# Performance work log

Hardware: AMD Instinct MI355X
Metric: run time of the kernel (lower is better)

## Reference

```python
import jax, jax.numpy as jnp
import numpy as np
from jax import lax

K = 3
PAD = 1


def setup_inputs() -> dict:
    key = jax.random.key(0)
    k1, k2, k3 = jax.random.split(key, 3)
    B, Cin, Cout, H, W = 4, 64, 64, 128, 128
    x = jax.random.normal(k1, (B, Cin, H, W), dtype=jnp.float32)
    # offset-predicting conv params (2*K*K output channels); small init keeps offsets modest
    offset_w = jax.random.normal(k2, (2 * K * K, Cin, K, K), dtype=jnp.float32) * 0.05
    offset_b = jnp.zeros((2 * K * K,), dtype=jnp.float32)
    # deformable conv weight/bias (module uses randn weight, zero bias)
    weight = jax.random.normal(k3, (Cout, Cin, K, K), dtype=jnp.float32) * 0.05
    bias = jnp.zeros((Cout,), dtype=jnp.float32)
    return {"x": x, "offset_w": offset_w, "offset_b": offset_b, "weight": weight, "bias": bias}


def _conv2d(x, w, b):
    y = lax.conv_general_dilated(x, w, window_strides=(1, 1),
                                 padding=((PAD, PAD), (PAD, PAD)),
                                 dimension_numbers=("NCHW", "OIHW", "NCHW"))
    return y + b[None, :, None, None]


def _bilinear_gather(x, py, px):
    # x: [B,C,H,W]; py,px: [B,KK,HO,WO] sample coords -> [B,C,KK,HO,WO], zeros outside
    B, C, H, W = x.shape
    y0 = jnp.floor(py)
    x0 = jnp.floor(px)
    ly = py - y0
    lx = px - x0
    y0i = y0.astype(jnp.int32)
    x0i = x0.astype(jnp.int32)
    xf = x.reshape(B, C, H * W)

    def corner(yi, xi, w):
        mask = ((yi >= 0) & (yi < H) & (xi >= 0) & (xi < W)).astype(x.dtype)
        lin = jnp.clip(yi, 0, H - 1) * W + jnp.clip(xi, 0, W - 1)  # [B,KK,HO,WO]
        g = jax.vmap(lambda xb, ib: xb[:, ib])(xf, lin)            # [B,C,KK,HO,WO]
        return g * (w * mask)[:, None]

    return (corner(y0i, x0i, (1 - ly) * (1 - lx))
            + corner(y0i, x0i + 1, (1 - ly) * lx)
            + corner(y0i + 1, x0i, ly * (1 - lx))
            + corner(y0i + 1, x0i + 1, ly * lx))


def reference(x, offset_w, offset_b, weight, bias):
    B, Cin, H, W = x.shape
    Cout = weight.shape[0]
    KK = K * K
    offset = _conv2d(x, offset_w, offset_b)            # [B, 2*KK, H, W]
    off = offset.reshape(B, KK, 2, H, W)               # torchvision layout: (dy, dx) per tap
    dy, dx = off[:, :, 0], off[:, :, 1]                # [B,KK,H,W]
    ki = (jnp.arange(KK) // K).astype(x.dtype)
    kj = (jnp.arange(KK) % K).astype(x.dtype)
    hs = jnp.arange(H, dtype=x.dtype)
    ws = jnp.arange(W, dtype=x.dtype)
    base_y = ki[:, None, None] + hs[None, :, None] - PAD   # [KK,H,1]
    base_x = kj[:, None, None] + ws[None, None, :] - PAD   # [KK,1,W]
    py = dy + base_y[None]                             # [B,KK,H,W]
    px = dx + base_x[None]
    sampled = _bilinear_gather(x, py, px)              # [B,Cin,KK,H,W]
    out = jnp.einsum("bckhw,ock->bohw", sampled, weight.reshape(Cout, Cin, KK))
    return out + bias[None, :, None, None]
```

## Files before the change

### kernel.cpp

```cpp
#include <hip/hip_runtime.h>

typedef _Float16 f16x8 __attribute__((ext_vector_type(8)));
typedef float f32x4 __attribute__((ext_vector_type(4)));

__device__ __forceinline__ f16x8 splat8(float v) {
  _Float16 h = (_Float16)v;
  return f16x8{h, h, h, h, h, h, h, h};
}

__global__ __launch_bounds__(256) void k_xtprep(const float* __restrict__ x,
                                                const float* __restrict__ wt,
                                                const float* __restrict__ ow,
                                                _Float16* __restrict__ xt,
                                                _Float16* __restrict__ wb,
                                                _Float16* __restrict__ owb) {
  __shared__ float tile[64 * 65];
  int blk = blockIdx.x;
  int t = threadIdx.x;
  if (blk < 1024) {
    int b = blk >> 8;
    int y = (blk >> 1) & 127;
    int w0 = (blk & 1) * 64;
    const float* xp = x + ((size_t)(b * 64) * 128 + y) * 128 + w0;
#pragma unroll
    for (int it = 0; it < 4; ++it) {
      int idx = it * 256 + t;
      int c = idx >> 4, q = idx & 15;
      float4 v = *(const float4*)(xp + (size_t)c * 16384 + q * 4);
      float* tp = &tile[c * 65 + q * 4];
      tp[0] = v.x; tp[1] = v.y; tp[2] = v.z; tp[3] = v.w;
    }
    __syncthreads();
#pragma unroll
    for (int it = 0; it < 2; ++it) {
      int idx = it * 256 + t;
      int w = idx >> 3, c8 = idx & 7;
      f16x8 o;
#pragma unroll
      for (int j = 0; j < 8; ++j) o[j] = (_Float16)tile[(c8 * 8 + j) * 65 + w];
      *(f16x8*)&xt[(((size_t)b * 128 + y) * 128 + w0 + w) * 64 + c8 * 8] = o;
    }
  } else {
    int i = (blk - 1024) * 256 + t;
    if (i < 36864) {
      int k = i >> 12, rem = i & 4095, o = rem >> 6, c = rem & 63;
      wb[i] = (_Float16)wt[(o * 64 + c) * 9 + k];
    } else if (i < 36864 + 18432) {
      int j = i - 36864;
      int k = j >> 11, rem = j & 2047, o = rem >> 6, c = rem & 63;
      float v = (o < 18) ? ow[(o * 64 + c) * 9 + k] : 0.0f;
      owb[j] = (_Float16)v;
    }
  }
}

__global__ __launch_bounds__(256, 4) void k_fused(
    const _Float16* __restrict__ xt, const _Float16* __restrict__ wb,
    const _Float16* __restrict__ owb, const float* __restrict__ ob,
    const float* __restrict__ bias, float* __restrict__ out) {
  __shared__ char lds[37728];
  _Float16* S = (_Float16*)lds;
  _Float16* WkL = (_Float16*)(lds + 9216);
  float* offL = (float*)(lds + 18432);
  _Float16* Xs = (_Float16*)lds;
  _Float16* owbkL = (_Float16*)(lds + 28512);

  int t = threadIdx.x;
  int lb = (blockIdx.x & 7) * 128 + (blockIdx.x >> 3);
  int w0 = (lb & 1) * 64;
  int h = (lb >> 1) & 127;
  int b = lb >> 8;

  int lane = t & 63, wid = t >> 6;
  int row = lane & 15, quad = lane >> 4;
  const _Float16* xb = xt + (size_t)b * 128 * 128 * 64;

#pragma unroll
  for (int it = 0; it < 8; ++it) {
    int idx8 = it * 256 + t;
    if (idx8 < 1584) {
      int c8 = idx8 & 7;
      int jr = idx8 >> 3;
      int jj = jr % 66;
      int ki = jr / 66;
      int gy = h - 1 + ki;
      int gx = w0 - 1 + jj;
      f16x8 v = {};
      if (((unsigned)gy < 128u) & ((unsigned)gx < 128u))
        v = *(const f16x8*)(xb + ((size_t)gy * 128 + gx) * 64 + c8 * 8);
      *(f16x8*)&Xs[(ki * 66 + jj) * 72 + c8 * 8] = v;
    } else if (idx8 < 1840) {
      int j = idx8 - 1584;
      int o = j >> 3, c8 = j & 7;
      *(f16x8*)&owbkL[o * 72 + c8 * 8] = *(const f16x8*)(owb + j * 8);
    }
  }
  __syncthreads();

  {
    int woA = (wid >> 1) * 16;
    int wpA = (wid & 1) * 32;
    f32x4 accA[2];
    accA[0] = f32x4{0.f, 0.f, 0.f, 0.f};
    accA[1] = f32x4{0.f, 0.f, 0.f, 0.f};
#pragma unroll
    for (int k = 0; k < 9; ++k) {
      if (k < 8) {
        int o = t >> 3, c8 = t & 7;
        *(f16x8*)&owbkL[((k + 1) & 1) * 2304 + o * 72 + c8 * 8] =
            *(const f16x8*)(owb + (k + 1) * 2048 + t * 8);
      }
      int ki = k / 3, kj = k % 3;
      const _Float16* ap = &owbkL[(k & 1) * 2304 + (woA + row) * 72 + quad * 8];
      f16x8 afr0 = *(const f16x8*)(ap);
      f16x8 afr1 = *(const f16x8*)(ap + 32);
#pragma unroll
      for (int n = 0; n < 2; ++n) {
        int j = wpA + n * 16 + row + kj;
        const _Float16* lp = &Xs[(ki * 66 + j) * 72 + quad * 8];
        f16x8 b0 = *(const f16x8*)(lp);
        f16x8 b1 = *(const f16x8*)(lp + 32);
        accA[n] = __builtin_amdgcn_mfma_f32_16x16x32_f16(afr0, b0, accA[n], 0, 0, 0);
        accA[n] = __builtin_amdgcn_mfma_f32_16x16x32_f16(afr1, b1, accA[n], 0, 0, 0);
      }
      __syncthreads();
    }
    int qr = quad * 4;
#pragma unroll
    for (int n = 0; n < 2; ++n) {
#pragma unroll
      for (int r = 0; r < 4; ++r) {
        int co = woA + qr + r;
        if (co < 18)
          offL[(wpA + n * 16 + row) * 20 + co] = accA[n][r] + ob[co];
      }
    }
  }
  __syncthreads();

  int pix = t >> 2, cg = t & 3;
  int w = w0 + pix;
  int woB = (wid >> 1) * 32, wpB = (wid & 1) * 32;

  f32x4 acc[2][2];
#pragma unroll
  for (int i = 0; i < 2; ++i)
#pragma unroll
    for (int j = 0; j < 2; ++j) acc[i][j] = f32x4{0.f, 0.f, 0.f, 0.f};

  for (int k = 0; k < 9; ++k) {
    {
      const f16x8* src = (const f16x8*)(wb + k * 4096);
#pragma unroll
      for (int r = 0; r < 2; ++r) {
        int idx8 = r * 256 + t;
        int o = idx8 >> 3, c8 = idx8 & 7;
        *(f16x8*)&WkL[o * 72 + c8 * 8] = src[idx8];
      }
    }
    {
      int ki = k / 3, kj = k % 3;
      float dy = offL[pix * 20 + 2 * k];
      float dx = offL[pix * 20 + 2 * k + 1];
      float py = dy + (float)(h + ki - 1);
      float pxf = dx + (float)(w + kj - 1);
      float fy = floorf(py), fx = floorf(pxf);
      float ly = py - fy, lx = pxf - fx;
      int y0 = (int)fy, x0 = (int)fx;
      int y1 = y0 + 1, x1 = x0 + 1;
      bool vy0 = (unsigned)y0 < 128u, vy1 = (unsigned)y1 < 128u;
      bool vx0 = (unsigned)x0 < 128u, vx1 = (unsigned)x1 < 128u;
      float w00 = (vy0 && vx0) ? (1.f - ly) * (1.f - lx) : 0.f;
      float w01 = (vy0 && vx1) ? (1.f - ly) * lx : 0.f;
      float w10 = (vy1 && vx0) ? ly * (1.f - lx) : 0.f;
      float w11 = (vy1 && vx1) ? ly * lx : 0.f;
      int yc0 = min(max(y0, 0), 127), yc1 = min(max(y1, 0), 127);
      int xc0 = min(max(x0, 0), 127), xc1 = min(max(x1, 0), 127);
      const _Float16* p00 = xb + (yc0 * 128 + xc0) * 64 + cg * 16;
      int dxo = (xc1 - xc0) * 64;
      int dyo = (yc1 - yc0) * 8192;
      f16x8 a0 = *(const f16x8*)(p00);
      f16x8 a1 = *(const f16x8*)(p00 + 8);
      f16x8 b0 = *(const f16x8*)(p00 + dxo);
      f16x8 b1 = *(const f16x8*)(p00 + dxo + 8);
      f16x8 c0v = *(const f16x8*)(p00 + dyo);
      f16x8 c1 = *(const f16x8*)(p00 + dyo + 8);
      f16x8 d0 = *(const f16x8*)(p00 + dyo + dxo);
      f16x8 d1 = *(const f16x8*)(p00 + dyo + dxo + 8);
      f16x8 W00 = splat8(w00), W01 = splat8(w01);
      f16x8 W10 = splat8(w10), W11 = splat8(w11);
      f16x8 s0 = W00 * a0 + W01 * b0 + W10 * c0v + W11 * d0;
      f16x8 s1 = W00 * a1 + W01 * b1 + W10 * c1 + W11 * d1;
      *(f16x8*)&S[pix * 72 + cg * 16] = s0;
      *(f16x8*)&S[pix * 72 + cg * 16 + 8] = s1;
    }
    __syncthreads();
    {
#pragma unroll
      for (int ks = 0; ks < 2; ++ks) {
        int c0 = ks * 32 + quad * 8;
        f16x8 afr[2], bfr[2];
#pragma unroll
        for (int mi = 0; mi < 2; ++mi)
          afr[mi] = *(const f16x8*)&WkL[(woB + mi * 16 + row) * 72 + c0];
#pragma unroll
        for (int ni = 0; ni < 2; ++ni)
          bfr[ni] = *(const f16x8*)&S[(wpB + ni * 16 + row) * 72 + c0];
#pragma unroll
        for (int mi = 0; mi < 2; ++mi)
#pragma unroll
          for (int ni = 0; ni < 2; ++ni)
            acc[mi][ni] = __builtin_amdgcn_mfma_f32_16x16x32_f16(
                afr[mi], bfr[ni], acc[mi][ni], 0, 0, 0);
      }
    }
    __syncthreads();
  }
  {
    int col = lane & 15;
    int qr = quad * 4;
#pragma unroll
    for (int mi = 0; mi < 2; ++mi) {
#pragma unroll
      for (int ni = 0; ni < 2; ++ni) {
#pragma unroll
        for (int r = 0; r < 4; ++r) {
          int o = woB + mi * 16 + qr + r;
          int pw = w0 + wpB + ni * 16 + col;
          out[(((size_t)b * 64 + o) * 128 + h) * 128 + pw] = acc[mi][ni][r] + bias[o];
        }
      }
    }
  }
}

extern "C" void kernel_launch(void* const* d_in, const int* in_sizes, int n_in,
                              void* d_out, int out_size, void* d_ws,
                              size_t ws_size, hipStream_t stream) {
  const float* x = (const float*)d_in[0];
  const float* ow = (const float*)d_in[1];
  const float* ob = (const float*)d_in[2];
  const float* wt = (const float*)d_in[3];
  const float* bias = (const float*)d_in[4];
  float* out = (float*)d_out;

  char* ws = (char*)d_ws;
  _Float16* xt = (_Float16*)ws;
  _Float16* wb = (_Float16*)(ws + 8388608);
  _Float16* owb = (_Float16*)(ws + 8388608 + 73728);

  k_xtprep<<<1240, 256, 0, stream>>>(x, wt, ow, xt, wb, owb);
  k_fused<<<1024, 256, 0, stream>>>(xt, wb, owb, ob, bias, out);
}
```

Before: 40.43 us.

## Software-pipeline deformable sampling and weight loads with double-buffered swizzled LDS

Restructures the main tap loop so the global gathers for tap k+1 and its weight slice are issued before the MFMA work of tap k, then blended and written into the other half of a double-buffered LDS region afterwards. This cuts one barrier per iteration and hides gather latency behind compute. LDS padding (stride 72) is replaced by an XOR swizzle on a stride-64 layout to avoid bank conflicts, and the loop is fully unrolled. In exchange, LDS grows to 40 KB and register pressure rises, which may limit occupancy under the 4-blocks launch bound.

```diff
diff --git a/kernel.cpp b/kernel.cpp
--- a/kernel.cpp
+++ b/kernel.cpp
@@ -7,6 +7,8 @@
   _Float16 h = (_Float16)v;
   return f16x8{h, h, h, h, h, h, h, h};
 }
+
+__device__ __forceinline__ int swzh(int i) { return i ^ (((i >> 6) & 7) << 3); }
 
 __global__ __launch_bounds__(256) void k_xtprep(const float* __restrict__ x,
                                                 const float* __restrict__ wt,
@@ -58,12 +60,12 @@
     const _Float16* __restrict__ xt, const _Float16* __restrict__ wb,
     const _Float16* __restrict__ owb, const float* __restrict__ ob,
     const float* __restrict__ bias, float* __restrict__ out) {
-  __shared__ char lds[37728];
-  _Float16* S = (_Float16*)lds;
-  _Float16* WkL = (_Float16*)(lds + 9216);
-  float* offL = (float*)(lds + 18432);
+  __shared__ char lds[40960];
+  _Float16* Sb = (_Float16*)lds;
+  _Float16* Wp = (_Float16*)(lds + 16384);
   _Float16* Xs = (_Float16*)lds;
-  _Float16* owbkL = (_Float16*)(lds + 28512);
+  _Float16* owbp = (_Float16*)(lds + 32768);
+  float* offL = (float*)(lds + 32768);
 
   int t = threadIdx.x;
   int lb = (blockIdx.x & 7) * 128 + (blockIdx.x >> 3);
@@ -92,7 +94,7 @@
     } else if (idx8 < 1840) {
       int j = idx8 - 1584;
       int o = j >> 3, c8 = j & 7;
-      *(f16x8*)&owbkL[o * 72 + c8 * 8] = *(const f16x8*)(owb + j * 8);
+      *(f16x8*)&owbp[swzh(o * 64 + c8 * 8)] = *(const f16x8*)(owb + j * 8);
     }
   }
   __syncthreads();
@@ -107,13 +109,13 @@
     for (int k = 0; k < 9; ++k) {
       if (k < 8) {
         int o = t >> 3, c8 = t & 7;
-        *(f16x8*)&owbkL[((k + 1) & 1) * 2304 + o * 72 + c8 * 8] =
-            *(const f16x8*)(owb + (k + 1) * 2048 + t * 8);
+        f16x8 v = *(const f16x8*)(owb + (k + 1) * 2048 + t * 8);
+        *(f16x8*)&owbp[swzh(((k + 1) & 1) * 2048 + o * 64 + c8 * 8)] = v;
       }
       int ki = k / 3, kj = k % 3;
-      const _Float16* ap = &owbkL[(k & 1) * 2304 + (woA + row) * 72 + quad * 8];
-      f16x8 afr0 = *(const f16x8*)(ap);
-      f16x8 afr1 = *(const f16x8*)(ap + 32);
+      int ai = (k & 1) * 2048 + (woA + row) * 64 + quad * 8;
+      f16x8 afr0 = *(const f16x8*)&owbp[swzh(ai)];
+      f16x8 afr1 = *(const f16x8*)&owbp[swzh(ai + 32)];
 #pragma unroll
       for (int n = 0; n < 2; ++n) {
         int j = wpA + n * 16 + row + kj;
@@ -142,70 +144,88 @@
   int w = w0 + pix;
   int woB = (wid >> 1) * 32, wpB = (wid & 1) * 32;
 
+  f16x8 wk0, wk1, ga0, ga1, gb0, gb1, gc0, gc1, gd0, gd1;
+  float w00, w01, w10, w11;
+
+#define SAMPLE_ISSUE(KK)                                                     \
+  {                                                                          \
+    float dy = offL[pix * 20 + 2 * (KK)];                                    \
+    float dx = offL[pix * 20 + 2 * (KK) + 1];                                \
+    float py = dy + (float)(h + (KK) / 3 - 1);                               \
+    float pxf = dx + (float)(w + (KK) % 3 - 1);                              \
+    float fy = floorf(py), fx = floorf(pxf);                                 \
+    float ly = py - fy, lx = pxf - fx;                                       \
+    int y0 = (int)fy, x0 = (int)fx;                                          \
+    int y1 = y0 + 1, x1 = x0 + 1;                                            \
+    bool vy0 = (unsigned)y0 < 128u, vy1 = (unsigned)y1 < 128u;               \
+    bool vx0 = (unsigned)x0 < 128u, vx1 = (unsigned)x1 < 128u;               \
+    w00 = (vy0 && vx0) ? (1.f - ly) * (1.f - lx) : 0.f;                      \
+    w01 = (vy0 && vx1) ? (1.f - ly) * lx : 0.f;                              \
+    w10 = (vy1 && vx0) ? ly * (1.f - lx) : 0.f;                              \
+    w11 = (vy1 && vx1) ? ly * lx : 0.f;                                      \
+    int yc0 = min(max(y0, 0), 127), yc1 = min(max(y1, 0), 127);              \
+    int xc0 = min(max(x0, 0), 127), xc1 = min(max(x1, 0), 127);              \
+    const _Float16* p00 = xb + (yc0 * 128 + xc0) * 64 + cg * 16;             \
+    int dxo = (xc1 - xc0) * 64, dyo = (yc1 - yc0) * 8192;                    \
+    ga0 = *(const f16x8*)(p00);                                              \
+    ga1 = *(const f16x8*)(p00 + 8);                                          \
+    gb0 = *(const f16x8*)(p00 + dxo);                                        \
+    gb1 = *(const f16x8*)(p00 + dxo + 8);                                    \
+    gc0 = *(const f16x8*)(p00 + dyo);                                        \
+    gc1 = *(const f16x8*)(p00 + dyo + 8);                                    \
+    gd0 = *(const f16x8*)(p00 + dyo + dxo);                                  \
+    gd1 = *(const f16x8*)(p00 + dyo + dxo + 8);                              \
+  }
+
+#define SAMPLE_FINISH(DSTBUF)                                                \
+  {                                                                          \
+    f16x8 W00 = splat8(w00), W01 = splat8(w01);                              \
+    f16x8 W10 = splat8(w10), W11 = splat8(w11);                              \
+    f16x8 s0 = W00 * ga0 + W01 * gb0 + W10 * gc0 + W11 * gd0;                \
+    f16x8 s1 = W00 * ga1 + W01 * gb1 + W10 * gc1 + W11 * gd1;                \
+    int si = (DSTBUF) * 4096 + pix * 64 + cg * 16;                           \
+    *(f16x8*)&Sb[swzh(si)] = s0;                                             \
+    *(f16x8*)&Sb[swzh(si + 8)] = s1;                                         \
+  }
+
   f32x4 acc[2][2];
 #pragma unroll
   for (int i = 0; i < 2; ++i)
 #pragma unroll
     for (int j = 0; j < 2; ++j) acc[i][j] = f32x4{0.f, 0.f, 0.f, 0.f};
 
+  {
+    const f16x8* wsrc = (const f16x8*)wb;
+    wk0 = wsrc[t];
+    wk1 = wsrc[256 + t];
+    SAMPLE_ISSUE(0)
+    SAMPLE_FINISH(0)
+    int wi = (t >> 3) * 64 + (t & 7) * 8;
+    *(f16x8*)&Wp[swzh(wi)] = wk0;
+    *(f16x8*)&Wp[swzh(wi + 2048)] = wk1;
+  }
+  __syncthreads();
+
+#pragma unroll
   for (int k = 0; k < 9; ++k) {
+    if (k < 8) {
+      const f16x8* wsrc = (const f16x8*)(wb + (k + 1) * 4096);
+      wk0 = wsrc[t];
+      wk1 = wsrc[256 + t];
+      SAMPLE_ISSUE(k + 1)
+    }
     {
-      const f16x8* src = (const f16x8*)(wb + k * 4096);
-#pragma unroll
-      for (int r = 0; r < 2; ++r) {
-        int idx8 = r * 256 + t;
-        int o = idx8 >> 3, c8 = idx8 & 7;
-        *(f16x8*)&WkL[o * 72 + c8 * 8] = src[idx8];
-      }
-    }
-    {
-      int ki = k / 3, kj = k % 3;
-      float dy = offL[pix * 20 + 2 * k];
-      float dx = offL[pix * 20 + 2 * k + 1];
-      float py = dy + (float)(h + ki - 1);
-      float pxf = dx + (float)(w + kj - 1);
-      float fy = floorf(py), fx = floorf(pxf);
-      float ly = py - fy, lx = pxf - fx;
-      int y0 = (int)fy, x0 = (int)fx;
-      int y1 = y0 + 1, x1 = x0 + 1;
-      bool vy0 = (unsigned)y0 < 128u, vy1 = (unsigned)y1 < 128u;
-      bool vx0 = (unsigned)x0 < 128u, vx1 = (unsigned)x1 < 128u;
-      float w00 = (vy0 && vx0) ? (1.f - ly) * (1.f - lx) : 0.f;
-      float w01 = (vy0 && vx1) ? (1.f - ly) * lx : 0.f;
-      float w10 = (vy1 && vx0) ? ly * (1.f - lx) : 0.f;
-      float w11 = (vy1 && vx1) ? ly * lx : 0.f;
-      int yc0 = min(max(y0, 0), 127), yc1 = min(max(y1, 0), 127);
-      int xc0 = min(max(x0, 0), 127), xc1 = min(max(x1, 0), 127);
-      const _Float16* p00 = xb + (yc0 * 128 + xc0) * 64 + cg * 16;
-      int dxo = (xc1 - xc0) * 64;
-      int dyo = (yc1 - yc0) * 8192;
-      f16x8 a0 = *(const f16x8*)(p00);
-      f16x8 a1 = *(const f16x8*)(p00 + 8);
-      f16x8 b0 = *(const f16x8*)(p00 + dxo);
-      f16x8 b1 = *(const f16x8*)(p00 + dxo + 8);
-      f16x8 c0v = *(const f16x8*)(p00 + dyo);
-      f16x8 c1 = *(const f16x8*)(p00 + dyo + 8);
-      f16x8 d0 = *(const f16x8*)(p00 + dyo + dxo);
-      f16x8 d1 = *(const f16x8*)(p00 + dyo + dxo + 8);
-      f16x8 W00 = splat8(w00), W01 = splat8(w01);
-      f16x8 W10 = splat8(w10), W11 = splat8(w11);
-      f16x8 s0 = W00 * a0 + W01 * b0 + W10 * c0v + W11 * d0;
-      f16x8 s1 = W00 * a1 + W01 * b1 + W10 * c1 + W11 * d1;
-      *(f16x8*)&S[pix * 72 + cg * 16] = s0;
-      *(f16x8*)&S[pix * 72 + cg * 16 + 8] = s1;
-    }
-    __syncthreads();
-    {
+      int bufo = (k & 1) * 4096;
 #pragma unroll
       for (int ks = 0; ks < 2; ++ks) {
         int c0 = ks * 32 + quad * 8;
         f16x8 afr[2], bfr[2];
 #pragma unroll
         for (int mi = 0; mi < 2; ++mi)
-          afr[mi] = *(const f16x8*)&WkL[(woB + mi * 16 + row) * 72 + c0];
+          afr[mi] = *(const f16x8*)&Wp[swzh(bufo + (woB + mi * 16 + row) * 64 + c0)];
 #pragma unroll
         for (int ni = 0; ni < 2; ++ni)
-          bfr[ni] = *(const f16x8*)&S[(wpB + ni * 16 + row) * 72 + c0];
+          bfr[ni] = *(const f16x8*)&Sb[swzh(bufo + (wpB + ni * 16 + row) * 64 + c0)];
 #pragma unroll
         for (int mi = 0; mi < 2; ++mi)
 #pragma unroll
@@ -214,8 +234,17 @@
                 afr[mi], bfr[ni], acc[mi][ni], 0, 0, 0);
       }
     }
-    __syncthreads();
-  }
+    if (k < 8) {
+      SAMPLE_FINISH((k + 1) & 1)
+      int wi = ((k + 1) & 1) * 4096 + (t >> 3) * 64 + (t & 7) * 8;
+      *(f16x8*)&Wp[swzh(wi)] = wk0;
+      *(f16x8*)&Wp[swzh(wi + 2048)] = wk1;
+      __syncthreads();
+    }
+  }
+#undef SAMPLE_ISSUE
+#undef SAMPLE_FINISH
+
   {
     int col = lane & 15;
     int qr = quad * 4;
```

Result: slower. 41.91 us (+3.6%).

## Retile fused deformable conv to 4x32 pixel blocks with swizzled LDS and batched weight loads

Applied to the files above, without the earlier changes.

The fused kernel now runs 512-thread blocks that each cover a 4-row by 32-column output tile, where before it used 256-thread blocks covering 1x64. The input halo needed for the offset conv shrinks relative to the output it serves. LDS padding is replaced with an XOR swizzle. Offset-conv and main-conv weights are staged three taps at a time in double buffers, which cuts the number of barriers per tap. The cost is more LDS per block (about 74KB), fewer resident blocks, and a less coalesced output store (32-wide rows).

```diff
diff --git a/kernel.cpp b/kernel.cpp
--- a/kernel.cpp
+++ b/kernel.cpp
@@ -7,6 +7,8 @@
   _Float16 h = (_Float16)v;
   return f16x8{h, h, h, h, h, h, h, h};
 }
+
+__device__ __forceinline__ int swzh(int i) { return i ^ (((i >> 6) & 7) << 3); }
 
 __global__ __launch_bounds__(256) void k_xtprep(const float* __restrict__ x,
                                                 const float* __restrict__ wt,
@@ -54,93 +56,110 @@
   }
 }
 
-__global__ __launch_bounds__(256, 4) void k_fused(
+__global__ __launch_bounds__(512, 2) void k_fused(
     const _Float16* __restrict__ xt, const _Float16* __restrict__ wb,
     const _Float16* __restrict__ owb, const float* __restrict__ ob,
     const float* __restrict__ bias, float* __restrict__ out) {
-  __shared__ char lds[37728];
-  _Float16* S = (_Float16*)lds;
-  _Float16* WkL = (_Float16*)(lds + 9216);
-  float* offL = (float*)(lds + 18432);
+  __shared__ char lds[75776];
+  _Float16* Wp3 = (_Float16*)lds;
+  _Float16* S = (_Float16*)(lds + 49152);
   _Float16* Xs = (_Float16*)lds;
-  _Float16* owbkL = (_Float16*)(lds + 28512);
+  _Float16* owbL = (_Float16*)(lds + 26112);
+  float* offL = (float*)(lds + 65536);
 
   int t = threadIdx.x;
-  int lb = (blockIdx.x & 7) * 128 + (blockIdx.x >> 3);
-  int w0 = (lb & 1) * 64;
-  int h = (lb >> 1) & 127;
-  int b = lb >> 8;
+  int lb = (blockIdx.x & 7) * 64 + (blockIdx.x >> 3);
+  int w0 = (lb & 3) * 32;
+  int h0 = ((lb >> 2) & 31) * 4;
+  int b = lb >> 7;
 
   int lane = t & 63, wid = t >> 6;
-  int row = lane & 15, quad = lane >> 4;
+  int lr = lane & 15, quad = lane >> 4;
   const _Float16* xb = xt + (size_t)b * 128 * 128 * 64;
 
 #pragma unroll
-  for (int it = 0; it < 8; ++it) {
-    int idx8 = it * 256 + t;
-    if (idx8 < 1584) {
+  for (int it = 0; it < 4; ++it) {
+    int idx8 = it * 512 + t;
+    if (idx8 < 1632) {
       int c8 = idx8 & 7;
       int jr = idx8 >> 3;
-      int jj = jr % 66;
-      int ki = jr / 66;
-      int gy = h - 1 + ki;
-      int gx = w0 - 1 + jj;
+      int col = jr % 34;
+      int xr = jr / 34;
+      int gy = h0 - 1 + xr;
+      int gx = w0 - 1 + col;
       f16x8 v = {};
       if (((unsigned)gy < 128u) & ((unsigned)gx < 128u))
         v = *(const f16x8*)(xb + ((size_t)gy * 128 + gx) * 64 + c8 * 8);
-      *(f16x8*)&Xs[(ki * 66 + jj) * 72 + c8 * 8] = v;
-    } else if (idx8 < 1840) {
-      int j = idx8 - 1584;
-      int o = j >> 3, c8 = j & 7;
-      *(f16x8*)&owbkL[o * 72 + c8 * 8] = *(const f16x8*)(owb + j * 8);
-    }
-  }
-  __syncthreads();
+      *(f16x8*)&Xs[swzh(jr * 64 + c8 * 8)] = v;
+    }
+  }
+#pragma unroll
+  for (int it = 0; it < 2; ++it) {
+    int idx8 = it * 512 + t;
+    if (idx8 < 768) {
+      int kb = idx8 >> 8, rem = idx8 & 255;
+      int o = rem >> 3, c8 = rem & 7;
+      *(f16x8*)&owbL[swzh(kb * 2048 + o * 64 + c8 * 8)] =
+          ((const f16x8*)(owb + kb * 2048))[rem];
+    }
+  }
 
   {
-    int woA = (wid >> 1) * 16;
-    int wpA = (wid & 1) * 32;
+    int oh = (wid >> 2) * 16;
+    int ar = wid & 3;
     f32x4 accA[2];
     accA[0] = f32x4{0.f, 0.f, 0.f, 0.f};
     accA[1] = f32x4{0.f, 0.f, 0.f, 0.f};
 #pragma unroll
-    for (int k = 0; k < 9; ++k) {
-      if (k < 8) {
-        int o = t >> 3, c8 = t & 7;
-        *(f16x8*)&owbkL[((k + 1) & 1) * 2304 + o * 72 + c8 * 8] =
-            *(const f16x8*)(owb + (k + 1) * 2048 + t * 8);
-      }
-      int ki = k / 3, kj = k % 3;
-      const _Float16* ap = &owbkL[(k & 1) * 2304 + (woA + row) * 72 + quad * 8];
-      f16x8 afr0 = *(const f16x8*)(ap);
-      f16x8 afr1 = *(const f16x8*)(ap + 32);
-#pragma unroll
-      for (int n = 0; n < 2; ++n) {
-        int j = wpA + n * 16 + row + kj;
-        const _Float16* lp = &Xs[(ki * 66 + j) * 72 + quad * 8];
-        f16x8 b0 = *(const f16x8*)(lp);
-        f16x8 b1 = *(const f16x8*)(lp + 32);
-        accA[n] = __builtin_amdgcn_mfma_f32_16x16x32_f16(afr0, b0, accA[n], 0, 0, 0);
-        accA[n] = __builtin_amdgcn_mfma_f32_16x16x32_f16(afr1, b1, accA[n], 0, 0, 0);
-      }
+    for (int bt = 0; bt < 3; ++bt) {
       __syncthreads();
+#pragma unroll
+      for (int kb = 0; kb < 3; ++kb) {
+        int ai = (bt & 1) * 6144 + kb * 2048 + (oh + lr) * 64 + quad * 8;
+        f16x8 afr0 = *(const f16x8*)&owbL[swzh(ai)];
+        f16x8 afr1 = *(const f16x8*)&owbL[swzh(ai + 32)];
+#pragma unroll
+        for (int ni = 0; ni < 2; ++ni) {
+          int j = ni * 16 + lr + kb;
+          int bi = ((ar + bt) * 34 + j) * 64 + quad * 8;
+          f16x8 b0 = *(const f16x8*)&Xs[swzh(bi)];
+          f16x8 b1 = *(const f16x8*)&Xs[swzh(bi + 32)];
+          accA[ni] = __builtin_amdgcn_mfma_f32_16x16x32_f16(afr0, b0, accA[ni], 0, 0, 0);
+          accA[ni] = __builtin_amdgcn_mfma_f32_16x16x32_f16(afr1, b1, accA[ni], 0, 0, 0);
+        }
+      }
+      if (bt < 2) {
+#pragma unroll
+        for (int it = 0; it < 2; ++it) {
+          int idx8 = it * 512 + t;
+          if (idx8 < 768) {
+            int kb = idx8 >> 8, rem = idx8 & 255;
+            int o = rem >> 3, c8 = rem & 7;
+            *(f16x8*)&owbL[swzh(((bt + 1) & 1) * 6144 + kb * 2048 + o * 64 + c8 * 8)] =
+                ((const f16x8*)(owb + ((bt + 1) * 3 + kb) * 2048))[rem];
+          }
+        }
+      }
     }
     int qr = quad * 4;
 #pragma unroll
-    for (int n = 0; n < 2; ++n) {
+    for (int ni = 0; ni < 2; ++ni) {
 #pragma unroll
       for (int r = 0; r < 4; ++r) {
-        int co = woA + qr + r;
-        if (co < 18)
-          offL[(wpA + n * 16 + row) * 20 + co] = accA[n][r] + ob[co];
+        int co = oh + qr + r;
+        if (co < 18) {
+          int px = ar * 32 + ni * 16 + lr;
+          offL[px * 20 + co] = accA[ni][r] + ob[co];
+        }
       }
     }
   }
   __syncthreads();
 
-  int pix = t >> 2, cg = t & 3;
-  int w = w0 + pix;
-  int woB = (wid >> 1) * 32, wpB = (wid & 1) * 32;
+  int pixS = t >> 2, cg = t & 3;
+  int rS = pixS >> 5;
+  int wS = w0 + (pixS & 31);
+  int woB = (wid >> 2) * 32, wpB = (wid & 3) * 32;
 
   f32x4 acc[2][2];
 #pragma unroll
@@ -148,22 +167,34 @@
 #pragma unroll
     for (int j = 0; j < 2; ++j) acc[i][j] = f32x4{0.f, 0.f, 0.f, 0.f};
 
+#pragma unroll
+  for (int it = 0; it < 3; ++it) {
+    int idx8 = it * 512 + t;
+    int kb = idx8 >> 9, rem = idx8 & 511;
+    int o = rem >> 3, c8 = rem & 7;
+    *(f16x8*)&Wp3[swzh(kb * 4096 + o * 64 + c8 * 8)] =
+        ((const f16x8*)(wb + kb * 4096))[rem];
+  }
+
+#pragma unroll
   for (int k = 0; k < 9; ++k) {
-    {
-      const f16x8* src = (const f16x8*)(wb + k * 4096);
-#pragma unroll
-      for (int r = 0; r < 2; ++r) {
-        int idx8 = r * 256 + t;
-        int o = idx8 >> 3, c8 = idx8 & 7;
-        *(f16x8*)&WkL[o * 72 + c8 * 8] = src[idx8];
+    if (k == 1 || k == 4) {
+      int bt = k / 3 + 1;
+#pragma unroll
+      for (int it = 0; it < 3; ++it) {
+        int idx8 = it * 512 + t;
+        int kb = idx8 >> 9, rem = idx8 & 511;
+        int o = rem >> 3, c8 = rem & 7;
+        *(f16x8*)&Wp3[swzh((bt & 1) * 12288 + kb * 4096 + o * 64 + c8 * 8)] =
+            ((const f16x8*)(wb + (bt * 3 + kb) * 4096))[rem];
       }
     }
     {
       int ki = k / 3, kj = k % 3;
-      float dy = offL[pix * 20 + 2 * k];
-      float dx = offL[pix * 20 + 2 * k + 1];
-      float py = dy + (float)(h + ki - 1);
-      float pxf = dx + (float)(w + kj - 1);
+      float dy = offL[pixS * 20 + 2 * k];
+      float dx = offL[pixS * 20 + 2 * k + 1];
+      float py = dy + (float)(h0 + rS + ki - 1);
+      float pxf = dx + (float)(wS + kj - 1);
       float fy = floorf(py), fx = floorf(pxf);
       float ly = py - fy, lx = pxf - fx;
       int y0 = (int)fy, x0 = (int)fx;
@@ -177,35 +208,36 @@
       int yc0 = min(max(y0, 0), 127), yc1 = min(max(y1, 0), 127);
       int xc0 = min(max(x0, 0), 127), xc1 = min(max(x1, 0), 127);
       const _Float16* p00 = xb + (yc0 * 128 + xc0) * 64 + cg * 16;
-      int dxo = (xc1 - xc0) * 64;
-      int dyo = (yc1 - yc0) * 8192;
-      f16x8 a0 = *(const f16x8*)(p00);
-      f16x8 a1 = *(const f16x8*)(p00 + 8);
-      f16x8 b0 = *(const f16x8*)(p00 + dxo);
-      f16x8 b1 = *(const f16x8*)(p00 + dxo + 8);
-      f16x8 c0v = *(const f16x8*)(p00 + dyo);
-      f16x8 c1 = *(const f16x8*)(p00 + dyo + 8);
-      f16x8 d0 = *(const f16x8*)(p00 + dyo + dxo);
-      f16x8 d1 = *(const f16x8*)(p00 + dyo + dxo + 8);
+      int dxo = (xc1 - xc0) * 64, dyo = (yc1 - yc0) * 8192;
+      f16x8 ga0 = *(const f16x8*)(p00);
+      f16x8 ga1 = *(const f16x8*)(p00 + 8);
+      f16x8 gb0 = *(const f16x8*)(p00 + dxo);
+      f16x8 gb1 = *(const f16x8*)(p00 + dxo + 8);
+      f16x8 gc0 = *(const f16x8*)(p00 + dyo);
+      f16x8 gc1 = *(const f16x8*)(p00 + dyo + 8);
+      f16x8 gd0 = *(const f16x8*)(p00 + dyo + dxo);
+      f16x8 gd1 = *(const f16x8*)(p00 + dyo + dxo + 8);
       f16x8 W00 = splat8(w00), W01 = splat8(w01);
       f16x8 W10 = splat8(w10), W11 = splat8(w11);
-      f16x8 s0 = W00 * a0 + W01 * b0 + W10 * c0v + W11 * d0;
-      f16x8 s1 = W00 * a1 + W01 * b1 + W10 * c1 + W11 * d1;
-      *(f16x8*)&S[pix * 72 + cg * 16] = s0;
-      *(f16x8*)&S[pix * 72 + cg * 16 + 8] = s1;
+      f16x8 s0 = W00 * ga0 + W01 * gb0 + W10 * gc0 + W11 * gd0;
+      f16x8 s1 = W00 * ga1 + W01 * gb1 + W10 * gc1 + W11 * gd1;
+      int si = pixS * 64 + cg * 16;
+      *(f16x8*)&S[swzh(si)] = s0;
+      *(f16x8*)&S[swzh(si + 8)] = s1;
     }
     __syncthreads();
     {
+      int wo = ((k / 3) & 1) * 12288 + (k % 3) * 4096;
 #pragma unroll
       for (int ks = 0; ks < 2; ++ks) {
         int c0 = ks * 32 + quad * 8;
-        f16x8 afr[2], bfr[2];
+        f16x8 bfr[2], afr[2];
+#pragma unroll
+        for (int ni = 0; ni < 2; ++ni)
+          bfr[ni] = *(const f16x8*)&S[swzh((wpB + ni * 16 + lr) * 64 + c0)];
 #pragma unroll
         for (int mi = 0; mi < 2; ++mi)
-          afr[mi] = *(const f16x8*)&WkL[(woB + mi * 16 + row) * 72 + c0];
-#pragma unroll
-        for (int ni = 0; ni < 2; ++ni)
-          bfr[ni] = *(const f16x8*)&S[(wpB + ni * 16 + row) * 72 + c0];
+          afr[mi] = *(const f16x8*)&Wp3[swzh(wo + (woB + mi * 16 + lr) * 64 + c0)];
 #pragma unroll
         for (int mi = 0; mi < 2; ++mi)
 #pragma unroll
@@ -214,8 +246,9 @@
                 afr[mi], bfr[ni], acc[mi][ni], 0, 0, 0);
       }
     }
-    __syncthreads();
-  }
+    if (k < 8) __syncthreads();
+  }
+
   {
     int col = lane & 15;
     int qr = quad * 4;
@@ -226,8 +259,9 @@
 #pragma unroll
         for (int r = 0; r < 4; ++r) {
           int o = woB + mi * 16 + qr + r;
-          int pw = w0 + wpB + ni * 16 + col;
-          out[(((size_t)b * 64 + o) * 128 + h) * 128 + pw] = acc[mi][ni][r] + bias[o];
+          int px = wpB + ni * 16 + col;
+          out[(((size_t)b * 64 + o) * 128 + h0 + (px >> 5)) * 128 + w0 + (px & 31)] =
+              acc[mi][ni][r] + bias[o];
         }
       }
     }
@@ -250,5 +284,5 @@
   _Float16* owb = (_Float16*)(ws + 8388608 + 73728);
 
   k_xtprep<<<1240, 256, 0, stream>>>(x, wt, ow, xt, wb, owb);
-  k_fused<<<1024, 256, 0, stream>>>(xt, wb, owb, ob, bias, out);
-}
+  k_fused<<<512, 512, 0, stream>>>(xt, wb, owb, ob, bias, out);
+}
```

New measurement: 35.82 us (median of 3 runs). 11.4% less time.
